# Performance work log

Hardware: AMD Instinct MI355X
Metric: run time of the kernel (lower is better)

The kernel has to match this reference:

```python
import jax, jax.numpy as jnp
import numpy as np

N_DIRS = 32  # number of projection directions


def gram_schmidt(x):
    # x: [B, n, D]; sequential Gram-Schmidt; normalized basis vectors are
    # detached (stop_gradient) as in the torch original.
    B, n, D = x.shape
    xs = jnp.swapaxes(x, 0, 1)  # [n, B, D]
    basis0 = jnp.zeros((n, B, D), dtype=x.dtype)

    def step(carry, w):
        basis, i = carry

        def proj(j, wv):
            b = basis[j]  # rows >= i are zero and contribute nothing
            return wv - b * jnp.sum(wv * b, axis=-1, keepdims=True)

        w_o = jax.lax.fori_loop(0, n, proj, w)
        w_sg = jax.lax.stop_gradient(w_o)
        w_hat = w_sg / jnp.linalg.norm(w_sg, axis=-1, keepdims=True)
        basis = jax.lax.dynamic_update_slice(basis, w_hat[None], (i, 0, 0))
        return (basis, i + 1), w_o

    (_, _), x_orth = jax.lax.scan(step, (basis0, jnp.int32(0)), xs)
    return jnp.swapaxes(x_orth, 0, 1)  # [B, n, D]


def setup_inputs() -> dict:
    key = jax.random.key(0)
    k = jax.random.split(key, 6)
    B = 2048
    IN_LP = 32 * 26       # 832 = linear_projection_x_dim * 26
    IMG = 28 * 28         # 784
    IN_NET = 2 * IMG      # 1568
    OUT_NET = N_DIRS * IMG  # 25088

    x_distorted = jax.random.normal(k[0], (B, IN_LP), dtype=jnp.float32)
    x_restored = jax.random.uniform(k[1], (B, 1, 28, 28), dtype=jnp.float32)

    s1 = 1.0 / np.sqrt(IN_LP)
    W_lp = jax.random.uniform(k[2], (IMG, IN_LP), jnp.float32, -s1, s1)
    b_lp = jax.random.uniform(k[3], (IMG,), jnp.float32, -s1, s1)

    s2 = 1.0 / np.sqrt(IN_NET)
    W_net = jax.random.uniform(k[4], (OUT_NET, IN_NET), jnp.float32, -s2, s2)
    b_net = jax.random.uniform(k[5], (OUT_NET,), jnp.float32, -s2, s2)

    return {"x_distorted": x_distorted, "x_restored": x_restored,
            "W_lp": W_lp, "b_lp": b_lp, "W_net": W_net, "b_net": b_net}


def reference(x_distorted, x_restored, W_lp, b_lp, W_net, b_net):
    B = x_distorted.shape[0]
    xd = x_distorted.reshape(B, -1) @ W_lp.T + b_lp      # [B, 784]
    xd = xd.reshape(B, 1, 28, 28)
    x = jnp.concatenate([xd, x_restored], axis=1)        # [B, 2, 28, 28]
    x = (x - 0.5) / 0.2
    w_mat = (x.reshape(B, -1) @ W_net.T + b_net) * 0.2   # [B, n_dirs*784]
    w_mat = w_mat.reshape(B, N_DIRS, -1)                 # [B, n_dirs, 784]
    return gram_schmidt(w_mat)
```

## Files before the change

### kernel.cpp

```cpp
#include <hip/hip_runtime.h>
#include <hip/hip_bf16.h>
#include <stdint.h>


typedef short s16x8 __attribute__((ext_vector_type(8)));
typedef float f32x4 __attribute__((ext_vector_type(4)));

#define GL_LDS16(gptr, lptr)                                                   \
    __builtin_amdgcn_global_load_lds(                                          \
        (const __attribute__((address_space(1))) void*)(gptr),                 \
        (__attribute__((address_space(3))) void*)(lptr), 16, 0, 0)

__global__ __launch_bounds__(512, 2) void gemm_mfma_256(
    const __hip_bfloat16* __restrict__ A, const __hip_bfloat16* __restrict__ B,
    const float* __restrict__ bias, float* __restrict__ C,
    int M, int N, int K)
{
    __shared__ __align__(16) short lds[4][16384];

    const int t = threadIdx.x;
    const int l = t & 63;
    const int wv = t >> 6;
    const int wm = wv >> 2;
    const int wn = wv & 3;

    const int f  = blockIdx.x;
    const int xb = f >> 3;
    const int yb = f & 7;
    const int m0 = yb * 256;
    const int n0 = xb * 256;

    const short* As = (const short*)A;
    const short* Bs = (const short*)B;

    const int colE = ((((l & 3) << 4) ^ ((l & 24) << 1)) >> 1);
    const size_t baseA0 = (size_t)(m0 + wv * 32 +  0 + (l >> 2)) * K + colE;
    const size_t baseA1 = (size_t)(m0 + wv * 32 + 16 + (l >> 2)) * K + colE;
    const size_t baseB0 = (size_t)(n0 + wv * 32 +  0 + (l >> 2)) * K + colE;
    const size_t baseB1 = (size_t)(n0 + wv * 32 + 16 + (l >> 2)) * K + colE;
    const int dst0 = (wv * 2 + 0) * 512;
    const int dst1 = (wv * 2 + 1) * 512;

    const int xk   = ((l >> 4) * 16) ^ ((l & 6) << 3);
    const int aoff = ((wm * 128 + (l & 15)) * 64 + xk) >> 1;
    const int boff = ((wn * 64  + (l & 15)) * 64 + xk) >> 1;

    f32x4 acc[8][4] = {};

#define STAGE_TILE(buf, T)                                                     \
    do {                                                                       \
        short* bA_ = &lds[buf][0];                                             \
        short* bB_ = &lds[buf][8192];                                          \
        const size_t ko_ = (size_t)(T) * 32;                                   \
        GL_LDS16(As + baseA0 + ko_, bA_ + dst0);                               \
        GL_LDS16(As + baseA1 + ko_, bA_ + dst1);                               \
        GL_LDS16(Bs + baseB0 + ko_, bB_ + dst0);                               \
        GL_LDS16(Bs + baseB1 + ko_, bB_ + dst1);                               \
    } while (0)

    const int NT = K >> 5;
    STAGE_TILE(0, 0);
    STAGE_TILE(1, 1);
    STAGE_TILE(2, 2);

    for (int kt = 0; kt < NT; ++kt) {
        const int cur = kt & 3;
        if (kt < NT - 2)      asm volatile("s_waitcnt vmcnt(8)");
        else if (kt == NT - 2) asm volatile("s_waitcnt vmcnt(4)");
        else                  asm volatile("s_waitcnt vmcnt(0)");
        __builtin_amdgcn_sched_barrier(0);
        asm volatile("" ::: "memory");
        __builtin_amdgcn_s_barrier();
        asm volatile("" ::: "memory");
        __builtin_amdgcn_sched_barrier(0);

        if (kt + 3 < NT) STAGE_TILE((kt + 3) & 3, kt + 3);

        const short* bA = &lds[cur][0];
        const short* bB = &lds[cur][8192];
        s16x8 af[8], bf[4];
        #pragma unroll
        for (int mi = 0; mi < 8; ++mi)
            af[mi] = *(const s16x8*)&bA[aoff + mi * 512];
        #pragma unroll
        for (int ni = 0; ni < 4; ++ni)
            bf[ni] = *(const s16x8*)&bB[boff + ni * 512];

        __builtin_amdgcn_s_setprio(1);
        #pragma unroll
        for (int mi = 0; mi < 8; ++mi)
            #pragma unroll
            for (int ni = 0; ni < 4; ++ni)
                acc[mi][ni] = __builtin_amdgcn_mfma_f32_16x16x32_bf16(
                    af[mi], bf[ni], acc[mi][ni], 0, 0, 0);
        __builtin_amdgcn_s_setprio(0);
    }
#undef STAGE_TILE

    const int row0 = m0 + wm * 128 + ((l >> 4) << 2);
    const int col0 = n0 + wn * 64 + (l & 15);
    #pragma unroll
    for (int ni = 0; ni < 4; ++ni) {
        const int n = col0 + ni * 16;
        const float bn = bias[n];
        #pragma unroll
        for (int mi = 0; mi < 8; ++mi) {
            const int r0 = row0 + mi * 16;
            #pragma unroll
            for (int r = 0; r < 4; ++r)
                C[(size_t)(r0 + r) * N + n] = (acc[mi][ni][r] + bn) * 0.2f;
        }
    }
}

__global__ __launch_bounds__(256) void f32_to_bf16(
    const float* __restrict__ in, __hip_bfloat16* __restrict__ out, int n4)
{
    int i = blockIdx.x * blockDim.x + threadIdx.x;
    const int stride = gridDim.x * blockDim.x;
    for (; i < n4; i += stride) {
        float4 v = ((const float4*)in)[i];
        __hip_bfloat16 o[4] = {
            __float2bfloat16(v.x), __float2bfloat16(v.y),
            __float2bfloat16(v.z), __float2bfloat16(v.w)};
        *(ushort4*)&out[(size_t)i * 4] = *(const ushort4*)o;
    }
}

#define TILE_M 64
#define TILE_N 64
#define TILE_K 16
#define LDS_STRIDE 72

__global__ __launch_bounds__(256) void gemm_nt_lp(
    const float* __restrict__ A, const float* __restrict__ B,
    const float* __restrict__ bias, __hip_bfloat16* __restrict__ C,
    int M, int N, int K, int ldc)
{
    __shared__ float As[TILE_K][LDS_STRIDE];
    __shared__ float Bsh[TILE_K][LDS_STRIDE];

    const int t  = threadIdx.x;
    const int tx = t & 15;
    const int ty = t >> 4;
    const int m0 = blockIdx.y * TILE_M;
    const int n0 = blockIdx.x * TILE_N;
    const int lrow = t >> 2;
    const int lk   = (t & 3) << 2;

    float acc[4][4] = {};

    for (int kt = 0; kt < K; kt += TILE_K) {
        float4 av = *(const float4*)(A + (size_t)(m0 + lrow) * K + kt + lk);
        float4 bv = make_float4(0.f, 0.f, 0.f, 0.f);
        if (n0 + lrow < N)
            bv = *(const float4*)(B + (size_t)(n0 + lrow) * K + kt + lk);

        __syncthreads();
        As[lk + 0][lrow] = av.x; As[lk + 1][lrow] = av.y;
        As[lk + 2][lrow] = av.z; As[lk + 3][lrow] = av.w;
        Bsh[lk + 0][lrow] = bv.x; Bsh[lk + 1][lrow] = bv.y;
        Bsh[lk + 2][lrow] = bv.z; Bsh[lk + 3][lrow] = bv.w;
        __syncthreads();

        #pragma unroll
        for (int k = 0; k < TILE_K; ++k) {
            float4 a = *(const float4*)&As[k][ty << 2];
            float4 b = *(const float4*)&Bsh[k][tx << 2];
            acc[0][0] += a.x * b.x; acc[0][1] += a.x * b.y;
            acc[0][2] += a.x * b.z; acc[0][3] += a.x * b.w;
            acc[1][0] += a.y * b.x; acc[1][1] += a.y * b.y;
            acc[1][2] += a.y * b.z; acc[1][3] += a.y * b.w;
            acc[2][0] += a.z * b.x; acc[2][1] += a.z * b.y;
            acc[2][2] += a.z * b.z; acc[2][3] += a.z * b.w;
            acc[3][0] += a.w * b.x; acc[3][1] += a.w * b.y;
            acc[3][2] += a.w * b.z; acc[3][3] += a.w * b.w;
        }
    }

    #pragma unroll
    for (int j = 0; j < 4; ++j) {
        int n = n0 + (tx << 2) + j;
        if (n < N) {
            float bn = bias[n];
            #pragma unroll
            for (int i = 0; i < 4; ++i) {
                float v = (acc[i][j] + bn - 0.5f) / 0.2f;
                C[(size_t)(m0 + (ty << 2) + i) * ldc + n] = __float2bfloat16(v);
            }
        }
    }
}

__global__ __launch_bounds__(256) void build_restored(
    const float* __restrict__ xr, __hip_bfloat16* __restrict__ x)
{
    const int b = blockIdx.x;
    const int t = threadIdx.x;
    if (t < 196) {
        float4 v = *(const float4*)(xr + (size_t)b * 784 + (t << 2));
        __hip_bfloat16 o[4] = {
            __float2bfloat16((v.x - 0.5f) / 0.2f),
            __float2bfloat16((v.y - 0.5f) / 0.2f),
            __float2bfloat16((v.z - 0.5f) / 0.2f),
            __float2bfloat16((v.w - 0.5f) / 0.2f)};
        *(ushort4*)&x[(size_t)b * 1568 + 784 + (t << 2)] = *(const ushort4*)o;
    }
}

#define GS_N 32
#define GS_D 784

__global__ __launch_bounds__(256, 4) void gram_solve(
    const float* __restrict__ out, float* __restrict__ Mws)
{
    __shared__ __align__(16) short Wc[GS_N * 64];
    __shared__ float Gs[GS_N][GS_N + 1];
    __shared__ float Ms[GS_N][GS_N + 1];
    __shared__ float Ld[GS_N];

    const int t = threadIdx.x;
    const int l = t & 63;
    const int w = t >> 6;
    const float* row0 = out + (size_t)blockIdx.x * (GS_N * GS_D);

    const int wr = w >> 1, wc2 = w & 1;
    const int ra = wr * 16 + (l & 15);
    const int rb = wc2 * 16 + (l & 15);
    const int kg = l >> 4;

    f32x4 acc = {};

    for (int k0 = 0; k0 < 832; k0 += 64) {
        #pragma unroll
        for (int hh = 0; hh < 2; ++hh) {
            const int h   = t + hh * 256;
            const int r   = h >> 4;
            const int hg  = h & 15;
            const int col = k0 + (hg << 2);
            ushort4 u = make_ushort4(0, 0, 0, 0);
            if (col < GS_D) {
                float4 v = *(const float4*)(row0 + r * GS_D + col);
                __hip_bfloat16 hb[4] = {
                    __float2bfloat16(v.x), __float2bfloat16(v.y),
                    __float2bfloat16(v.z), __float2bfloat16(v.w)};
                u = *(const ushort4*)hb;
            }
            const int gp = (hg >> 1) ^ (r & 7);
            *(ushort4*)&Wc[(r << 6) + (gp << 3) + ((hg & 1) << 2)] = u;
        }
        __syncthreads();

        #pragma unroll
        for (int s = 0; s < 2; ++s) {
            const int ga = ((s << 2) + kg) ^ (ra & 7);
            const int gb = ((s << 2) + kg) ^ (rb & 7);
            s16x8 af = *(const s16x8*)&Wc[(ra << 6) + (ga << 3)];
            s16x8 bf = *(const s16x8*)&Wc[(rb << 6) + (gb << 3)];
            acc = __builtin_amdgcn_mfma_f32_16x16x32_bf16(af, bf, acc, 0, 0, 0);
        }
        __syncthreads();
    }

    {
        const int di = wr * 16 + (l >> 4) * 4;
        const int dj = wc2 * 16 + (l & 15);
        #pragma unroll
        for (int r = 0; r < 4; ++r) Gs[di + r][dj] = acc[r];
    }
    for (int z = t; z < GS_N * (GS_N + 1); z += 256) ((float*)Ms)[z] = 0.f;
    __syncthreads();

    for (int k = 0; k < GS_N; ++k) {
        const float sk = sqrtf(Gs[k][k]);
        if (t == k) Ld[k] = sk;
        if (t > k && t < GS_N) Gs[t][k] /= sk;
        __syncthreads();
        if (t > k && t < GS_N) {
            const float lik = Gs[t][k];
            for (int j = k + 1; j <= t; ++j)
                Gs[t][j] -= lik * Gs[j][k];
        }
        __syncthreads();
    }

    if (t < GS_N) {
        const int j = t;
        Ms[j][j] = 1.0f / Ld[j];
        for (int i = j + 1; i < GS_N; ++i) {
            float a = 0.f;
            for (int k = j; k < i; ++k)
                a += Gs[i][k] * Ms[k][j];
            Ms[i][j] = -a / Ld[i];
        }
        for (int i = j + 1; i < GS_N; ++i)
            Ms[i][j] *= Ld[i];
    }
    __syncthreads();

    {
        const int i = t >> 3, j0 = (t & 7) << 2;
        float4 mv = make_float4(Ms[i][j0], Ms[i][j0 + 1],
                                Ms[i][j0 + 2], Ms[i][j0 + 3]);
        *(float4*)(Mws + (size_t)blockIdx.x * 1024 + (t << 2)) = mv;
    }
}

__global__ __launch_bounds__(256, 8) void gs_apply(
    float* __restrict__ out, const float* __restrict__ Mws)
{
    __shared__ float4 Wf[GS_N][28];
    __shared__ float  Ml[GS_N][36];

    const int t = threadIdx.x;
    const int b = blockIdx.y;
    const int k0 = blockIdx.x * 112;
    float* row0 = out + (size_t)b * (GS_N * GS_D);

    {
        float4 mv = *(const float4*)(Mws + (size_t)b * 1024 + (t << 2));
        const int i = t >> 3, j0 = (t & 7) << 2;
        *(float4*)&Ml[i][j0] = mv;
    }
    #pragma unroll
    for (int hh = 0; hh < 4; ++hh) {
        const int h = t + hh * 256;
        const int r = h >> 5, c = h & 31;
        if (c < 28)
            Wf[r][c] = *(const float4*)(row0 + r * GS_D + k0 + (c << 2));
    }
    __syncthreads();

    const int rg = t >> 5;
    const int c4 = t & 31;
    if (c4 < 28) {
        const int i0 = rg << 2;
        float4 c0 = Wf[i0 + 0][c4];
        float4 c1 = Wf[i0 + 1][c4];
        float4 c2 = Wf[i0 + 2][c4];
        float4 c3 = Wf[i0 + 3][c4];
        for (int j = 0; j < GS_N - 1; ++j) {
            if (j > i0 + 2) break;
            const float4 wj = Wf[j][c4];
            const float m0 = (i0 + 0 > j) ? Ml[i0 + 0][j] : 0.f;
            const float m1 = (i0 + 1 > j) ? Ml[i0 + 1][j] : 0.f;
            const float m2 = (i0 + 2 > j) ? Ml[i0 + 2][j] : 0.f;
            const float m3 = (i0 + 3 > j) ? Ml[i0 + 3][j] : 0.f;
            c0.x += m0 * wj.x; c0.y += m0 * wj.y;
            c0.z += m0 * wj.z; c0.w += m0 * wj.w;
            c1.x += m1 * wj.x; c1.y += m1 * wj.y;
            c1.z += m1 * wj.z; c1.w += m1 * wj.w;
            c2.x += m2 * wj.x; c2.y += m2 * wj.y;
            c2.z += m2 * wj.z; c2.w += m2 * wj.w;
            c3.x += m3 * wj.x; c3.y += m3 * wj.y;
            c3.z += m3 * wj.z; c3.w += m3 * wj.w;
        }
        *(float4*)(row0 + (i0 + 0) * GS_D + k0 + (c4 << 2)) = c0;
        *(float4*)(row0 + (i0 + 1) * GS_D + k0 + (c4 << 2)) = c1;
        *(float4*)(row0 + (i0 + 2) * GS_D + k0 + (c4 << 2)) = c2;
        *(float4*)(row0 + (i0 + 3) * GS_D + k0 + (c4 << 2)) = c3;
    }
}

extern "C" void kernel_launch(void* const* d_in, const int* in_sizes, int n_in,
                              void* d_out, int out_size, void* d_ws, size_t ws_size,
                              hipStream_t stream)
{
    const float* xd   = (const float*)d_in[0];
    const float* xr   = (const float*)d_in[1];
    const float* Wlp  = (const float*)d_in[2];
    const float* blp  = (const float*)d_in[3];
    const float* Wnet = (const float*)d_in[4];
    const float* bnet = (const float*)d_in[5];
    float* out = (float*)d_out;

    const int B = 2048, IN_LP = 832, IMG = 784, IN_NET = 1568, OUT = 32 * 784;

    __hip_bfloat16* Wnet_bf = (__hip_bfloat16*)d_ws;
    __hip_bfloat16* x_bf =
        (__hip_bfloat16*)((char*)d_ws + (size_t)OUT * IN_NET * 2);
    float* Mws = (float*)d_ws;

    f32_to_bf16<<<2048, 256, 0, stream>>>(Wnet, Wnet_bf, OUT * IN_NET / 4);

    gemm_nt_lp<<<dim3((IMG + TILE_N - 1) / TILE_N, B / TILE_M), 256, 0, stream>>>(
        xd, Wlp, blp, x_bf, B, IMG, IN_LP, IN_NET);

    build_restored<<<B, 256, 0, stream>>>(xr, x_bf);

    gemm_mfma_256<<<dim3(784), 512, 0, stream>>>(
        x_bf, Wnet_bf, bnet, out, B, OUT, IN_NET);

    gram_solve<<<B, 256, 0, stream>>>(out, Mws);

    gs_apply<<<dim3(7, B), 256, 0, stream>>>(out, Mws);
}
```

Baseline: 463.8 us.

## Pad K to 1600 and switch main GEMM to K=64 double-buffered tiles

Pads the K dimension of both bf16 operands from 1568 to 1600 with zeros so the main GEMM can step through K in 64-wide tiles with a new swizzled LDS layout. The pipeline goes from four buffers of K=32 to two buffers of K=64 with __syncthreads, which halves the number of barriers per K. Occupancy drops from 2 to 1 blocks per CU and the loop does about 2% more padded MACs. The weight conversion becomes a per-row kernel that writes into the padded layout.

```diff
diff --git a/kernel.cpp b/kernel.cpp
--- a/kernel.cpp
+++ b/kernel.cpp
@@ -11,12 +11,14 @@
         (const __attribute__((address_space(1))) void*)(gptr),                 \
         (__attribute__((address_space(3))) void*)(lptr), 16, 0, 0)
 
-__global__ __launch_bounds__(512, 2) void gemm_mfma_256(
+#define KP 1600
+
+__global__ __launch_bounds__(512, 1) void gemm_mfma_256(
     const __hip_bfloat16* __restrict__ A, const __hip_bfloat16* __restrict__ B,
     const float* __restrict__ bias, float* __restrict__ C,
     int M, int N, int K)
 {
-    __shared__ __align__(16) short lds[4][16384];
+    __shared__ __align__(16) short lds[2][32768];
 
     const int t = threadIdx.x;
     const int l = t & 63;
@@ -33,67 +35,79 @@
     const short* As = (const short*)A;
     const short* Bs = (const short*)B;
 
-    const int colE = ((((l & 3) << 4) ^ ((l & 24) << 1)) >> 1);
-    const size_t baseA0 = (size_t)(m0 + wv * 32 +  0 + (l >> 2)) * K + colE;
-    const size_t baseA1 = (size_t)(m0 + wv * 32 + 16 + (l >> 2)) * K + colE;
-    const size_t baseB0 = (size_t)(n0 + wv * 32 +  0 + (l >> 2)) * K + colE;
-    const size_t baseB1 = (size_t)(n0 + wv * 32 + 16 + (l >> 2)) * K + colE;
-    const int dst0 = (wv * 2 + 0) * 512;
-    const int dst1 = (wv * 2 + 1) * 512;
-
-    const int xk   = ((l >> 4) * 16) ^ ((l & 6) << 3);
-    const int aoff = ((wm * 128 + (l & 15)) * 64 + xk) >> 1;
-    const int boff = ((wn * 64  + (l & 15)) * 64 + xk) >> 1;
+    const int colE = (((l & 7) ^ (l >> 3)) << 3);
+    const size_t aSrc0 = (size_t)(m0 +   0 + wv * 8 + (l >> 3)) * KP + colE;
+    const size_t aSrc1 = (size_t)(m0 + 128 + wv * 8 + (l >> 3)) * KP + colE;
+    const size_t bSrc0 = (size_t)(n0 +   0 + wv * 8 + (l >> 3)) * KP + colE;
+    const size_t bSrc1 = (size_t)(n0 + 128 + wv * 8 + (l >> 3)) * KP + colE;
+    const int dstW = wv * 512;
+
+    const int sk0 = (((l >> 4) << 3)) ^ ((l & 7) << 3);
+    const int sk1 = sk0 ^ 32;
+    const int aBase = wm * 8192 + (l & 15) * 64;
+    const int bBase = 16384 + (wn >> 1) * 8192 +
+                      ((wn & 1) * 64 + (l & 15)) * 64;
 
     f32x4 acc[8][4] = {};
 
 #define STAGE_TILE(buf, T)                                                     \
     do {                                                                       \
-        short* bA_ = &lds[buf][0];                                             \
-        short* bB_ = &lds[buf][8192];                                          \
-        const size_t ko_ = (size_t)(T) * 32;                                   \
-        GL_LDS16(As + baseA0 + ko_, bA_ + dst0);                               \
-        GL_LDS16(As + baseA1 + ko_, bA_ + dst1);                               \
-        GL_LDS16(Bs + baseB0 + ko_, bB_ + dst0);                               \
-        GL_LDS16(Bs + baseB1 + ko_, bB_ + dst1);                               \
+        short* d_ = &lds[buf][0];                                              \
+        const size_t ko_ = (size_t)(T) * 64;                                   \
+        GL_LDS16(As + aSrc0 + ko_,            d_ + dstW);                      \
+        GL_LDS16(As + aSrc0 + 64 * KP + ko_,  d_ + dstW + 4096);               \
+        GL_LDS16(As + aSrc1 + ko_,            d_ + dstW + 8192);               \
+        GL_LDS16(As + aSrc1 + 64 * KP + ko_,  d_ + dstW + 12288);              \
+        GL_LDS16(Bs + bSrc0 + ko_,            d_ + dstW + 16384);              \
+        GL_LDS16(Bs + bSrc0 + 64 * KP + ko_,  d_ + dstW + 20480);              \
+        GL_LDS16(Bs + bSrc1 + ko_,            d_ + dstW + 24576);              \
+        GL_LDS16(Bs + bSrc1 + 64 * KP + ko_,  d_ + dstW + 28672);              \
     } while (0)
 
-    const int NT = K >> 5;
+    const int NT = K >> 6;
     STAGE_TILE(0, 0);
-    STAGE_TILE(1, 1);
-    STAGE_TILE(2, 2);
+    __syncthreads();
 
     for (int kt = 0; kt < NT; ++kt) {
-        const int cur = kt & 3;
-        if (kt < NT - 2)      asm volatile("s_waitcnt vmcnt(8)");
-        else if (kt == NT - 2) asm volatile("s_waitcnt vmcnt(4)");
-        else                  asm volatile("s_waitcnt vmcnt(0)");
-        __builtin_amdgcn_sched_barrier(0);
-        asm volatile("" ::: "memory");
-        __builtin_amdgcn_s_barrier();
-        asm volatile("" ::: "memory");
-        __builtin_amdgcn_sched_barrier(0);
-
-        if (kt + 3 < NT) STAGE_TILE((kt + 3) & 3, kt + 3);
-
-        const short* bA = &lds[cur][0];
-        const short* bB = &lds[cur][8192];
-        s16x8 af[8], bf[4];
-        #pragma unroll
-        for (int mi = 0; mi < 8; ++mi)
-            af[mi] = *(const s16x8*)&bA[aoff + mi * 512];
-        #pragma unroll
-        for (int ni = 0; ni < 4; ++ni)
-            bf[ni] = *(const s16x8*)&bB[boff + ni * 512];
-
-        __builtin_amdgcn_s_setprio(1);
-        #pragma unroll
-        for (int mi = 0; mi < 8; ++mi)
+        const int cur = kt & 1;
+        const short* bufc = &lds[cur][0];
+
+        if (kt + 1 < NT) STAGE_TILE(cur ^ 1, kt + 1);
+
+        s16x8 bfr[4][2];
+        #pragma unroll
+        for (int ni = 0; ni < 4; ++ni) {
+            bfr[ni][0] = *(const s16x8*)&bufc[bBase + ni * 1024 + sk0];
+            bfr[ni][1] = *(const s16x8*)&bufc[bBase + ni * 1024 + sk1];
+        }
+
+        #pragma unroll
+        for (int half = 0; half < 2; ++half) {
+            s16x8 afr[4][2];
             #pragma unroll
-            for (int ni = 0; ni < 4; ++ni)
-                acc[mi][ni] = __builtin_amdgcn_mfma_f32_16x16x32_bf16(
-                    af[mi], bf[ni], acc[mi][ni], 0, 0, 0);
-        __builtin_amdgcn_s_setprio(0);
+            for (int mi = 0; mi < 4; ++mi) {
+                const int ro = (half * 64 + mi * 16) * 64;
+                afr[mi][0] = *(const s16x8*)&bufc[aBase + ro + sk0];
+                afr[mi][1] = *(const s16x8*)&bufc[aBase + ro + sk1];
+            }
+            __builtin_amdgcn_s_setprio(1);
+            #pragma unroll
+            for (int mi = 0; mi < 4; ++mi)
+                #pragma unroll
+                for (int ni = 0; ni < 4; ++ni) {
+                    acc[half * 4 + mi][ni] =
+                        __builtin_amdgcn_mfma_f32_16x16x32_bf16(
+                            afr[mi][0], bfr[ni][0], acc[half * 4 + mi][ni],
+                            0, 0, 0);
+                    acc[half * 4 + mi][ni] =
+                        __builtin_amdgcn_mfma_f32_16x16x32_bf16(
+                            afr[mi][1], bfr[ni][1], acc[half * 4 + mi][ni],
+                            0, 0, 0);
+                }
+            __builtin_amdgcn_s_setprio(0);
+        }
+
+        __syncthreads();
     }
 #undef STAGE_TILE
 
@@ -113,18 +127,23 @@
     }
 }
 
-__global__ __launch_bounds__(256) void f32_to_bf16(
-    const float* __restrict__ in, __hip_bfloat16* __restrict__ out, int n4)
-{
-    int i = blockIdx.x * blockDim.x + threadIdx.x;
-    const int stride = gridDim.x * blockDim.x;
-    for (; i < n4; i += stride) {
-        float4 v = ((const float4*)in)[i];
+__global__ __launch_bounds__(256) void wnet_to_bf16(
+    const float* __restrict__ in, __hip_bfloat16* __restrict__ out)
+{
+    const size_t r = blockIdx.x;
+    const int t = threadIdx.x;
+    const float* src = in + r * 1568;
+    __hip_bfloat16* dst = out + r * KP;
+
+    for (int i = t; i < 392; i += 256) {
+        float4 v = *(const float4*)(src + (i << 2));
         __hip_bfloat16 o[4] = {
             __float2bfloat16(v.x), __float2bfloat16(v.y),
             __float2bfloat16(v.z), __float2bfloat16(v.w)};
-        *(ushort4*)&out[(size_t)i * 4] = *(const ushort4*)o;
-    }
+        *(ushort4*)&dst[i << 2] = *(const ushort4*)o;
+    }
+    if (t < 8)
+        *(ushort4*)&dst[1568 + (t << 2)] = make_ushort4(0, 0, 0, 0);
 }
 
 #define TILE_M 64
@@ -204,7 +223,10 @@
             __float2bfloat16((v.y - 0.5f) / 0.2f),
             __float2bfloat16((v.z - 0.5f) / 0.2f),
             __float2bfloat16((v.w - 0.5f) / 0.2f)};
-        *(ushort4*)&x[(size_t)b * 1568 + 784 + (t << 2)] = *(const ushort4*)o;
+        *(ushort4*)&x[(size_t)b * KP + 784 + (t << 2)] = *(const ushort4*)o;
+    } else if (t < 204) {
+        *(ushort4*)&x[(size_t)b * KP + 1568 + ((t - 196) << 2)] =
+            make_ushort4(0, 0, 0, 0);
     }
 }
 
@@ -374,22 +396,22 @@
     const float* bnet = (const float*)d_in[5];
     float* out = (float*)d_out;
 
-    const int B = 2048, IN_LP = 832, IMG = 784, IN_NET = 1568, OUT = 32 * 784;
+    const int B = 2048, IN_LP = 832, IMG = 784, OUT = 32 * 784;
 
     __hip_bfloat16* Wnet_bf = (__hip_bfloat16*)d_ws;
     __hip_bfloat16* x_bf =
-        (__hip_bfloat16*)((char*)d_ws + (size_t)OUT * IN_NET * 2);
+        (__hip_bfloat16*)((char*)d_ws + (size_t)OUT * KP * 2);
     float* Mws = (float*)d_ws;
 
-    f32_to_bf16<<<2048, 256, 0, stream>>>(Wnet, Wnet_bf, OUT * IN_NET / 4);
+    wnet_to_bf16<<<OUT, 256, 0, stream>>>(Wnet, Wnet_bf);
 
     gemm_nt_lp<<<dim3((IMG + TILE_N - 1) / TILE_N, B / TILE_M), 256, 0, stream>>>(
-        xd, Wlp, blp, x_bf, B, IMG, IN_LP, IN_NET);
+        xd, Wlp, blp, x_bf, B, IMG, IN_LP, KP);
 
     build_restored<<<B, 256, 0, stream>>>(xr, x_bf);
 
     gemm_mfma_256<<<dim3(784), 512, 0, stream>>>(
-        x_bf, Wnet_bf, bnet, out, B, OUT, IN_NET);
+        x_bf, Wnet_bf, bnet, out, B, OUT, KP);
 
     gram_solve<<<B, 256, 0, stream>>>(out, Mws);
 
```

Result: no change. 455.7 us (-1.7%).
